# Kernel optimization log

Measured on AMD Instinct MI355X. Metric: run time of the kernel, lower is better.

Reference implementation:

```python
import jax, jax.numpy as jnp
import numpy as np


def setup_inputs() -> dict:
    key = jax.random.key(0)
    k1, k2 = jax.random.split(key)
    B, N, M = 8, 4096, 4096
    xyz1 = jax.random.normal(k1, (B, N, 3), dtype=jnp.float32)
    xyz2 = jax.random.normal(k2, (B, M, 3), dtype=jnp.float32)
    return {"xyz1": xyz1, "xyz2": xyz2}


def _chamfer_sq_dists(xyz1, xyz2):
    # Squared euclidean all-pairs distances via ||a||^2 + ||b||^2 - 2 a.b
    # xyz1: [B,N,3], xyz2: [B,M,3]
    n1 = jnp.sum(xyz1 * xyz1, axis=-1)              # [B,N]
    n2 = jnp.sum(xyz2 * xyz2, axis=-1)              # [B,M]
    dots = jnp.einsum('bnd,bmd->bnm', xyz1, xyz2)   # [B,N,M]
    d2 = n1[:, :, None] + n2[:, None, :] - 2.0 * dots
    dist1 = jnp.min(d2, axis=2)                     # [B,N] min over xyz2
    dist2 = jnp.min(d2, axis=1)                     # [B,M] min over xyz1
    return dist1, dist2


def reference(xyz1, xyz2):
    dist1, dist2 = _chamfer_sq_dists(xyz1, xyz2)
    return jnp.mean(dist1) + jnp.mean(dist2)
```

## Files before the change

kernel.cpp:

```cpp
#include <hip/hip_runtime.h>

typedef float f32x16 __attribute__((ext_vector_type(16)));
typedef short bf16x8 __attribute__((ext_vector_type(8)));

#define BLOCK 256
#define NPTS 4096
#define SEGS 32
#define SCANSPLIT 2
#define SCANPTS (NPTS / SCANSPLIT)
#define CHUNK 256
#define NCHUNK (SCANPTS / CHUNK)
#define SUBS (CHUNK / 32)

__device__ inline unsigned int f2bf(float x) {
    unsigned int u = __float_as_uint(x);
    return (u + 0x7FFFu + ((u >> 16) & 1)) >> 16;
}
__device__ inline float bf2f(unsigned int b) { return __uint_as_float(b << 16); }
__device__ inline unsigned int pk2(unsigned int lo, unsigned int hi) {
    return (hi << 16) | (lo & 0xFFFFu);
}
__device__ inline unsigned int fkey(float f) {
    unsigned int u = __float_as_uint(f);
    return (u & 0x80000000u) ? ~u : (u | 0x80000000u);
}
__device__ inline float funkey(unsigned int k) {
    unsigned int u = (k & 0x80000000u) ? (k & 0x7FFFFFFFu) : ~k;
    return __uint_as_float(u);
}

__global__ __launch_bounds__(BLOCK) void pack_pts(
    const float* __restrict__ x1, const float* __restrict__ x2,
    uint4* __restrict__ arrA, uint4* __restrict__ arrB,
    float* __restrict__ wn, unsigned int* __restrict__ mins,
    int n1, int ntot, float* __restrict__ out) {
    int i = blockIdx.x * BLOCK + threadIdx.x;
    if (i == 0) out[0] = 0.0f;
    if (i >= ntot) return;
    const float* s = (i < n1) ? x1 + 3 * (size_t)i : x2 + 3 * (size_t)(i - n1);
    float x = s[0], y = s[1], z = s[2];
    float w = fmaf(z, z, fmaf(y, y, x * x));
    wn[i] = w;
    mins[i] = 0xFFFFFFFFu;
    unsigned int hx = f2bf(x), hy = f2bf(y), hz = f2bf(z);
    unsigned int lx = f2bf(x - bf2f(hx)), ly = f2bf(y - bf2f(hy)), lz = f2bf(z - bf2f(hz));
    unsigned int hw = f2bf(w), lw = f2bf(w - bf2f(hw));
    unsigned int ax = f2bf(-2.f * bf2f(hx)), ay = f2bf(-2.f * bf2f(hy)), az = f2bf(-2.f * bf2f(hz));
    unsigned int bx = f2bf(-2.f * bf2f(lx)), by = f2bf(-2.f * bf2f(ly)), bz = f2bf(-2.f * bf2f(lz));
    const unsigned int one = 0x3F80u;
    arrA[(size_t)i * 2 + 0] = make_uint4(pk2(ax, ay), pk2(az, bx), pk2(by, bz), pk2(ax, ay));
    arrA[(size_t)i * 2 + 1] = make_uint4(pk2(az, one), pk2(one, 0u), 0u, 0u);
    arrB[(size_t)i * 2 + 0] = make_uint4(pk2(hx, hy), pk2(hz, hx), pk2(hy, hz), pk2(lx, ly));
    arrB[(size_t)i * 2 + 1] = make_uint4(pk2(lz, hw), pk2(lw, 0u), 0u, 0u);
}

__global__ __launch_bounds__(BLOCK) void chamfer_mfma(
    const uint4* __restrict__ arrA, const uint4* __restrict__ arrB,
    unsigned int* __restrict__ mins, int n1, int Bc) {
    __shared__ uint4 lds[2][2][CHUNK];
    int tid = threadIdx.x;
    int lane = tid & 63, widx = tid >> 6;
    int l31 = lane & 31, blk = lane >> 5;

    int bid = blockIdx.x;
    int sh = bid % SCANSPLIT;
    int t1 = bid / SCANSPLIT;
    int seg = t1 % SEGS;
    int bd = t1 / SEGS;
    int dir = (bd >= Bc) ? 1 : 0;
    int b = dir ? bd - Bc : bd;
    int ownOff = dir ? n1 : 0;
    int othOff = dir ? 0 : n1;

    int row0 = seg * 128 + widx * 32;

    size_t aBase = (size_t)(ownOff + b * NPTS + row0 + l31) * 2 + blk;
    bf16x8 afA = *(const bf16x8*)(arrA + aBase);

    const uint4* gB = arrB + (size_t)(othOff + b * NPTS + sh * SCANPTS) * 2;

    f32x16 run;
#pragma unroll
    for (int r = 0; r < 16; ++r) run[r] = 3.0e38f;

    uint4 u0 = gB[tid], u1 = gB[tid + 256];
    lds[0][tid & 1][tid >> 1] = u0;
    lds[0][tid & 1][128 + (tid >> 1)] = u1;
    __syncthreads();

    f32x16 zero = {};
    for (int c = 0; c < NCHUNK; ++c) {
        int cur = c & 1;
        if (c + 1 < NCHUNK) {
            u0 = gB[(c + 1) * 512 + tid];
            u1 = gB[(c + 1) * 512 + 256 + tid];
        }
        const uint4* lp = lds[cur][blk];
#pragma unroll
        for (int s = 0; s < SUBS; s += 2) {
            bf16x8 bf0 = *(const bf16x8*)(lp + s * 32 + l31);
            bf16x8 bf1 = *(const bf16x8*)(lp + (s + 1) * 32 + l31);
            f32x16 acc0 = __builtin_amdgcn_mfma_f32_32x32x16_bf16(afA, bf0, zero, 0, 0, 0);
            f32x16 acc1 = __builtin_amdgcn_mfma_f32_32x32x16_bf16(afA, bf1, zero, 0, 0, 0);
#pragma unroll
            for (int r = 0; r < 16; ++r)
                run[r] = fminf(run[r], fminf(acc0[r], acc1[r]));
        }
        if (c + 1 < NCHUNK) {
            lds[cur ^ 1][tid & 1][tid >> 1] = u0;
            lds[cur ^ 1][tid & 1][128 + (tid >> 1)] = u1;
        }
        __syncthreads();
    }

#pragma unroll
    for (int m = 1; m <= 16; m <<= 1)
#pragma unroll
        for (int r = 0; r < 16; ++r)
            run[r] = fminf(run[r], __shfl_xor(run[r], m, 64));

    if (l31 == 0) {
        unsigned int* mo = mins + ownOff + b * NPTS;
#pragma unroll
        for (int r = 0; r < 16; ++r) {
            int row = row0 + ((r & 3) + 8 * (r >> 2) + 4 * blk);
            atomicMin(mo + row, fkey(run[r]));
        }
    }
}

__global__ __launch_bounds__(BLOCK) void reduce_means(
    const unsigned int* __restrict__ mins, const float* __restrict__ wn,
    int n1, int ntot, float inv1, float inv2, float* __restrict__ out) {
    float s = 0.0f;
    for (int i = blockIdx.x * BLOCK + threadIdx.x; i < ntot; i += gridDim.x * BLOCK) {
        float v = funkey(mins[i]) + wn[i];
        s += v * (i < n1 ? inv1 : inv2);
    }
    for (int off = 32; off; off >>= 1) s += __shfl_down(s, off, 64);
    __shared__ float red[BLOCK / 64];
    int lane = threadIdx.x & 63, wid = threadIdx.x >> 6;
    if (!lane) red[wid] = s;
    __syncthreads();
    if (!threadIdx.x) atomicAdd(out, red[0] + red[1] + red[2] + red[3]);
}

__global__ __launch_bounds__(BLOCK) void chamfer_direct(
    const float* __restrict__ x1, const float* __restrict__ x2,
    int Npts, int Mpts, float inv1, float inv2, float* __restrict__ out) {
    int dir = blockIdx.z;
    const float* own = dir ? x2 : x1;
    const float* oth = dir ? x1 : x2;
    int np = dir ? Mpts : Npts;
    int mp = dir ? Npts : Mpts;
    float scale = dir ? inv2 : inv1;

    int bpb = np / BLOCK;
    int b = blockIdx.x / bpb;
    int i = (blockIdx.x % bpb) * BLOCK + threadIdx.x;

    const float* pp = own + ((size_t)b * np + i) * 3;
    float px = pp[0], py = pp[1], pz = pp[2];
    const float* o = oth + (size_t)b * mp * 3;

    float best = 3.0e38f;
#pragma unroll 4
    for (int j = 0; j < mp; ++j) {
        float dx = px - o[3 * j + 0];
        float dy = py - o[3 * j + 1];
        float dz = pz - o[3 * j + 2];
        float d2 = fmaf(dz, dz, fmaf(dy, dy, dx * dx));
        best = fminf(best, d2);
    }
    float s = best * scale;
    for (int off = 32; off; off >>= 1) s += __shfl_down(s, off, 64);
    __shared__ float red[BLOCK / 64];
    int lane = threadIdx.x & 63, wid = threadIdx.x >> 6;
    if (!lane) red[wid] = s;
    __syncthreads();
    if (!threadIdx.x) atomicAdd(out, red[0] + red[1] + red[2] + red[3]);
}

extern "C" void kernel_launch(void* const* d_in, const int* in_sizes, int n_in,
                              void* d_out, int out_size, void* d_ws, size_t ws_size,
                              hipStream_t stream) {
    const float* xyz1 = (const float*)d_in[0];
    const float* xyz2 = (const float*)d_in[1];
    float* out = (float*)d_out;

    const int Bc = in_sizes[0] / (3 * NPTS);
    const int n1 = Bc * NPTS;
    const int n2 = Bc * NPTS;
    const int ntot = n1 + n2;

    size_t need = (size_t)ntot * (32 + 32 + 4 + 4);
    bool okShape = Bc >= 1 && in_sizes[0] == Bc * 3 * NPTS && in_sizes[1] == in_sizes[0];

    if (okShape && ws_size >= need) {
        uint4* arrA = (uint4*)d_ws;
        uint4* arrB = (uint4*)((char*)d_ws + (size_t)ntot * 32);
        float* wn = (float*)((char*)d_ws + (size_t)ntot * 64);
        unsigned int* mins = (unsigned int*)((char*)d_ws + (size_t)ntot * 68);

        pack_pts<<<(ntot + BLOCK - 1) / BLOCK, BLOCK, 0, stream>>>(
            xyz1, xyz2, arrA, arrB, wn, mins, n1, ntot, out);

        chamfer_mfma<<<Bc * 2 * SEGS * SCANSPLIT, BLOCK, 0, stream>>>(
            arrA, arrB, mins, n1, Bc);

        reduce_means<<<64, BLOCK, 0, stream>>>(mins, wn, n1, ntot,
                                               1.0f / (float)n1, 1.0f / (float)n2, out);
    } else {
        hipMemsetAsync(d_out, 0, sizeof(float), stream);
        dim3 grid((in_sizes[0] / 3 / NPTS) * (NPTS / BLOCK), 1, 2);
        chamfer_direct<<<grid, BLOCK, 0, stream>>>(xyz1, xyz2, NPTS, NPTS,
                                                   1.0f / (float)n1, 1.0f / (float)n2, out);
    }
}
```

Baseline: 39.48 us.

## Fuse packing, MFMA min-scan and mean reduction into one kernel

Replaces the three-kernel pipeline (pack to workspace, MFMA scan with atomicMin, reduce) with one kernel. Each block converts its own points and the streamed opposite points to split-bf16 form in registers and LDS on the fly. It also drops the scan split so every block sees all 4096 points, which lets it finish the row minimum locally and add to the output directly. This removes two launches, the workspace traffic and the atomicMin pass. In exchange the grid is half the size (512 blocks) and the bf16 conversion is recomputed redundantly by every block.

```diff
diff --git a/kernel.cpp b/kernel.cpp
--- a/kernel.cpp
+++ b/kernel.cpp
@@ -6,10 +6,8 @@
 #define BLOCK 256
 #define NPTS 4096
 #define SEGS 32
-#define SCANSPLIT 2
-#define SCANPTS (NPTS / SCANSPLIT)
 #define CHUNK 256
-#define NCHUNK (SCANPTS / CHUNK)
+#define NCHUNK (NPTS / CHUNK)
 #define SUBS (CHUNK / 32)
 
 __device__ inline unsigned int f2bf(float x) {
@@ -20,80 +18,70 @@
 __device__ inline unsigned int pk2(unsigned int lo, unsigned int hi) {
     return (hi << 16) | (lo & 0xFFFFu);
 }
-__device__ inline unsigned int fkey(float f) {
-    unsigned int u = __float_as_uint(f);
-    return (u & 0x80000000u) ? ~u : (u | 0x80000000u);
-}
-__device__ inline float funkey(unsigned int k) {
-    unsigned int u = (k & 0x80000000u) ? (k & 0x7FFFFFFFu) : ~k;
-    return __uint_as_float(u);
-}
 
-__global__ __launch_bounds__(BLOCK) void pack_pts(
+__global__ __launch_bounds__(BLOCK) void chamfer_fused(
     const float* __restrict__ x1, const float* __restrict__ x2,
-    uint4* __restrict__ arrA, uint4* __restrict__ arrB,
-    float* __restrict__ wn, unsigned int* __restrict__ mins,
-    int n1, int ntot, float* __restrict__ out) {
-    int i = blockIdx.x * BLOCK + threadIdx.x;
-    if (i == 0) out[0] = 0.0f;
-    if (i >= ntot) return;
-    const float* s = (i < n1) ? x1 + 3 * (size_t)i : x2 + 3 * (size_t)(i - n1);
-    float x = s[0], y = s[1], z = s[2];
-    float w = fmaf(z, z, fmaf(y, y, x * x));
-    wn[i] = w;
-    mins[i] = 0xFFFFFFFFu;
-    unsigned int hx = f2bf(x), hy = f2bf(y), hz = f2bf(z);
-    unsigned int lx = f2bf(x - bf2f(hx)), ly = f2bf(y - bf2f(hy)), lz = f2bf(z - bf2f(hz));
-    unsigned int hw = f2bf(w), lw = f2bf(w - bf2f(hw));
-    unsigned int ax = f2bf(-2.f * bf2f(hx)), ay = f2bf(-2.f * bf2f(hy)), az = f2bf(-2.f * bf2f(hz));
-    unsigned int bx = f2bf(-2.f * bf2f(lx)), by = f2bf(-2.f * bf2f(ly)), bz = f2bf(-2.f * bf2f(lz));
-    const unsigned int one = 0x3F80u;
-    arrA[(size_t)i * 2 + 0] = make_uint4(pk2(ax, ay), pk2(az, bx), pk2(by, bz), pk2(ax, ay));
-    arrA[(size_t)i * 2 + 1] = make_uint4(pk2(az, one), pk2(one, 0u), 0u, 0u);
-    arrB[(size_t)i * 2 + 0] = make_uint4(pk2(hx, hy), pk2(hz, hx), pk2(hy, hz), pk2(lx, ly));
-    arrB[(size_t)i * 2 + 1] = make_uint4(pk2(lz, hw), pk2(lw, 0u), 0u, 0u);
-}
+    int Bc, float inv1, float inv2, float* __restrict__ out) {
+    __shared__ uint4 lds[2][2][CHUNK];
+    __shared__ float wslot[128];
+    __shared__ float red[4];
 
-__global__ __launch_bounds__(BLOCK) void chamfer_mfma(
-    const uint4* __restrict__ arrA, const uint4* __restrict__ arrB,
-    unsigned int* __restrict__ mins, int n1, int Bc) {
-    __shared__ uint4 lds[2][2][CHUNK];
     int tid = threadIdx.x;
     int lane = tid & 63, widx = tid >> 6;
     int l31 = lane & 31, blk = lane >> 5;
 
     int bid = blockIdx.x;
-    int sh = bid % SCANSPLIT;
-    int t1 = bid / SCANSPLIT;
-    int seg = t1 % SEGS;
-    int bd = t1 / SEGS;
+    int seg = bid % SEGS;
+    int bd = bid / SEGS;
     int dir = (bd >= Bc) ? 1 : 0;
     int b = dir ? bd - Bc : bd;
-    int ownOff = dir ? n1 : 0;
-    int othOff = dir ? 0 : n1;
+    const float* own = dir ? x2 : x1;
+    const float* oth = dir ? x1 : x2;
+    float inv = dir ? inv2 : inv1;
 
     int row0 = seg * 128 + widx * 32;
 
-    size_t aBase = (size_t)(ownOff + b * NPTS + row0 + l31) * 2 + blk;
-    bf16x8 afA = *(const bf16x8*)(arrA + aBase);
+    bf16x8 afA;
+    {
+        const float* p = own + ((size_t)b * NPTS + row0 + l31) * 3;
+        float x = p[0], y = p[1], z = p[2];
+        float w = fmaf(z, z, fmaf(y, y, x * x));
+        unsigned int hx = f2bf(x), hy = f2bf(y), hz = f2bf(z);
+        unsigned int lx = f2bf(x - bf2f(hx)), ly = f2bf(y - bf2f(hy)), lz = f2bf(z - bf2f(hz));
+        unsigned int ax = f2bf(-2.f * bf2f(hx)), ay = f2bf(-2.f * bf2f(hy)), az = f2bf(-2.f * bf2f(hz));
+        unsigned int bx = f2bf(-2.f * bf2f(lx)), by = f2bf(-2.f * bf2f(ly)), bz = f2bf(-2.f * bf2f(lz));
+        const unsigned int one = 0x3F80u;
+        uint4 A0 = make_uint4(pk2(ax, ay), pk2(az, bx), pk2(by, bz), pk2(ax, ay));
+        uint4 A1 = make_uint4(pk2(az, one), pk2(one, 0u), 0u, 0u);
+        uint4 af4 = blk ? A1 : A0;
+        afA = *(const bf16x8*)&af4;
+        if (!blk) wslot[widx * 32 + l31] = w;
+    }
 
-    const uint4* gB = arrB + (size_t)(othOff + b * NPTS + sh * SCANPTS) * 2;
+    const float* os = oth + (size_t)b * NPTS * 3;
+    {
+        const float* q = os + (size_t)tid * 3;
+        float x = q[0], y = q[1], z = q[2];
+        float w = fmaf(z, z, fmaf(y, y, x * x));
+        unsigned int hx = f2bf(x), hy = f2bf(y), hz = f2bf(z);
+        unsigned int lx = f2bf(x - bf2f(hx)), ly = f2bf(y - bf2f(hy)), lz = f2bf(z - bf2f(hz));
+        unsigned int hw = f2bf(w), lw = f2bf(w - bf2f(hw));
+        lds[0][0][tid] = make_uint4(pk2(hx, hy), pk2(hz, hx), pk2(hy, hz), pk2(lx, ly));
+        lds[0][1][tid] = make_uint4(pk2(lz, hw), pk2(lw, 0u), 0u, 0u);
+    }
+    __syncthreads();
 
     f32x16 run;
 #pragma unroll
     for (int r = 0; r < 16; ++r) run[r] = 3.0e38f;
 
-    uint4 u0 = gB[tid], u1 = gB[tid + 256];
-    lds[0][tid & 1][tid >> 1] = u0;
-    lds[0][tid & 1][128 + (tid >> 1)] = u1;
-    __syncthreads();
-
     f32x16 zero = {};
     for (int c = 0; c < NCHUNK; ++c) {
         int cur = c & 1;
+        float nx, ny, nz;
         if (c + 1 < NCHUNK) {
-            u0 = gB[(c + 1) * 512 + tid];
-            u1 = gB[(c + 1) * 512 + 256 + tid];
+            const float* q = os + (size_t)((c + 1) * CHUNK + tid) * 3;
+            nx = q[0]; ny = q[1]; nz = q[2];
         }
         const uint4* lp = lds[cur][blk];
 #pragma unroll
@@ -107,8 +95,12 @@
                 run[r] = fminf(run[r], fminf(acc0[r], acc1[r]));
         }
         if (c + 1 < NCHUNK) {
-            lds[cur ^ 1][tid & 1][tid >> 1] = u0;
-            lds[cur ^ 1][tid & 1][128 + (tid >> 1)] = u1;
+            float w = fmaf(nz, nz, fmaf(ny, ny, nx * nx));
+            unsigned int hx = f2bf(nx), hy = f2bf(ny), hz = f2bf(nz);
+            unsigned int lx = f2bf(nx - bf2f(hx)), ly = f2bf(ny - bf2f(hy)), lz = f2bf(nz - bf2f(hz));
+            unsigned int hw = f2bf(w), lw = f2bf(w - bf2f(hw));
+            lds[cur ^ 1][0][tid] = make_uint4(pk2(hx, hy), pk2(hz, hx), pk2(hy, hz), pk2(lx, ly));
+            lds[cur ^ 1][1][tid] = make_uint4(pk2(lz, hw), pk2(lw, 0u), 0u, 0u);
         }
         __syncthreads();
     }
@@ -119,30 +111,18 @@
         for (int r = 0; r < 16; ++r)
             run[r] = fminf(run[r], __shfl_xor(run[r], m, 64));
 
+    float contrib = 0.0f;
     if (l31 == 0) {
-        unsigned int* mo = mins + ownOff + b * NPTS;
 #pragma unroll
         for (int r = 0; r < 16; ++r) {
-            int row = row0 + ((r & 3) + 8 * (r >> 2) + 4 * blk);
-            atomicMin(mo + row, fkey(run[r]));
+            int lrow = (r & 3) + 8 * (r >> 2) + 4 * blk;
+            contrib += run[r] + wslot[widx * 32 + lrow];
         }
     }
-}
-
-__global__ __launch_bounds__(BLOCK) void reduce_means(
-    const unsigned int* __restrict__ mins, const float* __restrict__ wn,
-    int n1, int ntot, float inv1, float inv2, float* __restrict__ out) {
-    float s = 0.0f;
-    for (int i = blockIdx.x * BLOCK + threadIdx.x; i < ntot; i += gridDim.x * BLOCK) {
-        float v = funkey(mins[i]) + wn[i];
-        s += v * (i < n1 ? inv1 : inv2);
-    }
-    for (int off = 32; off; off >>= 1) s += __shfl_down(s, off, 64);
-    __shared__ float red[BLOCK / 64];
-    int lane = threadIdx.x & 63, wid = threadIdx.x >> 6;
-    if (!lane) red[wid] = s;
+    contrib += __shfl_xor(contrib, 32, 64);
+    if (lane == 0) red[widx] = contrib * inv;
     __syncthreads();
-    if (!threadIdx.x) atomicAdd(out, red[0] + red[1] + red[2] + red[3]);
+    if (tid == 0) atomicAdd(out, red[0] + red[1] + red[2] + red[3]);
 }
 
 __global__ __launch_bounds__(BLOCK) void chamfer_direct(
@@ -191,27 +171,14 @@
     const int Bc = in_sizes[0] / (3 * NPTS);
     const int n1 = Bc * NPTS;
     const int n2 = Bc * NPTS;
-    const int ntot = n1 + n2;
-
-    size_t need = (size_t)ntot * (32 + 32 + 4 + 4);
     bool okShape = Bc >= 1 && in_sizes[0] == Bc * 3 * NPTS && in_sizes[1] == in_sizes[0];
 
-    if (okShape && ws_size >= need) {
-        uint4* arrA = (uint4*)d_ws;
-        uint4* arrB = (uint4*)((char*)d_ws + (size_t)ntot * 32);
-        float* wn = (float*)((char*)d_ws + (size_t)ntot * 64);
-        unsigned int* mins = (unsigned int*)((char*)d_ws + (size_t)ntot * 68);
+    hipMemsetAsync(d_out, 0, sizeof(float), stream);
 
-        pack_pts<<<(ntot + BLOCK - 1) / BLOCK, BLOCK, 0, stream>>>(
-            xyz1, xyz2, arrA, arrB, wn, mins, n1, ntot, out);
-
-        chamfer_mfma<<<Bc * 2 * SEGS * SCANSPLIT, BLOCK, 0, stream>>>(
-            arrA, arrB, mins, n1, Bc);
-
-        reduce_means<<<64, BLOCK, 0, stream>>>(mins, wn, n1, ntot,
-                                               1.0f / (float)n1, 1.0f / (float)n2, out);
+    if (okShape) {
+        chamfer_fused<<<Bc * 2 * SEGS, BLOCK, 0, stream>>>(
+            xyz1, xyz2, Bc, 1.0f / (float)n1, 1.0f / (float)n2, out);
     } else {
-        hipMemsetAsync(d_out, 0, sizeof(float), stream);
         dim3 grid((in_sizes[0] / 3 / NPTS) * (NPTS / BLOCK), 1, 2);
         chamfer_direct<<<grid, BLOCK, 0, stream>>>(xyz1, xyz2, NPTS, NPTS,
                                                    1.0f / (float)n1, 1.0f / (float)n2, out);
```

Result: faster. 38.21 us (median of 2 runs) (-3.2%).
